# Optimization experiments

Hardware: AMD Instinct MI355X
Metric: run time of the kernel (lower is better)

## Reference

```python
import jax, jax.numpy as jnp
import numpy as np

B, S, DIM, NH = 4, 2048, 2048, 16
HD = DIM // NH  # 128


def setup_inputs() -> dict:
    key = jax.random.key(0)
    ks = jax.random.split(key, 6)
    x = jax.random.normal(ks[0], (B, S, DIM), dtype=jnp.float32)
    wq = jax.random.normal(ks[1], (DIM, DIM), dtype=jnp.float32) * (DIM ** -0.5)
    wk = jax.random.normal(ks[2], (DIM, DIM), dtype=jnp.float32) * (DIM ** -0.5)
    wv = jax.random.normal(ks[3], (DIM, DIM), dtype=jnp.float32) * (DIM ** -0.5)
    wo = jax.random.normal(ks[4], (DIM, DIM), dtype=jnp.float32) * (DIM ** -0.5)
    # RoPE frequencies: theta^{-2i/hd}, angle = pos * freq
    inv_freq = 1.0 / (10000.0 ** (np.arange(0, HD, 2, dtype=np.float32) / HD))  # [HD/2]
    angles = np.arange(S, dtype=np.float32)[:, None] * inv_freq[None, :]  # [S, HD/2]
    freqs_cos = jnp.asarray(np.cos(angles))
    freqs_sin = jnp.asarray(np.sin(angles))
    # causal mask, additive [S, S]
    mask = jnp.where(jnp.tril(jnp.ones((S, S), dtype=bool)), 0.0, -jnp.inf).astype(jnp.float32)
    return {"x": x, "wq": wq, "wk": wk, "wv": wv, "wo": wo,
            "freqs_cos": freqs_cos, "freqs_sin": freqs_sin, "mask": mask,
            "start_pos": 0}


def _apply_rotary(xq, xk, cos, sin):
    # xq, xk: [B, S, H, HD]; cos/sin: [S, HD/2]
    def rot(t):
        tr = t.reshape(*t.shape[:-1], -1, 2)  # [B,S,H,HD/2,2]
        a, b = tr[..., 0], tr[..., 1]
        c = cos[None, :, None, :]
        s = sin[None, :, None, :]
        # complex multiply (a+ib)(c+is)
        out = jnp.stack([a * c - b * s, a * s + b * c], axis=-1)
        return out.reshape(t.shape)
    return rot(xq), rot(xk)


def reference(x, wq, wk, wv, wo, freqs_cos, freqs_sin, mask, start_pos):
    bsz, seqlen, _ = x.shape
    # nn.Linear: y = x @ W^T
    xq = (x @ wq.T).reshape(bsz, seqlen, NH, HD)
    xk = (x @ wk.T).reshape(bsz, seqlen, NH, HD)
    xv = (x @ wv.T).reshape(bsz, seqlen, NH, HD)
    xq, xk = _apply_rotary(xq, xk, freqs_cos, freqs_sin)
    # attention, heads to axis 1
    scores = jnp.einsum('bqhd,bkhd->bhqk', xq, xk) / jnp.sqrt(jnp.float32(HD))
    scores = scores + mask[None, None, :, :]
    probs = jax.nn.softmax(scores.astype(jnp.float32), axis=-1).astype(xq.dtype)
    out = jnp.einsum('bhqk,bkhd->bqhd', probs, xv).reshape(bsz, seqlen, -1)
    return out @ wo.T
```

## Files before the change

### kernel.cpp

```cpp
#include <hip/hip_runtime.h>

typedef __attribute__((ext_vector_type(8))) __bf16 bf16x8;
typedef __attribute__((ext_vector_type(4))) float f32x4;
typedef __attribute__((ext_vector_type(16))) float f32x16;
typedef __attribute__((ext_vector_type(8))) unsigned short u16x8;
typedef __attribute__((ext_vector_type(2))) unsigned uint2v;

#define LOG2E 1.44269504088896340736f

__device__ __forceinline__ unsigned short f2bf(float f){
  union { float f; unsigned u; } v; v.f = f;
  unsigned r = v.u + 0x7FFFu + ((v.u >> 16) & 1u);
  return (unsigned short)(r >> 16);
}
__device__ __forceinline__ float bf2f(unsigned short u){
  union { unsigned u; float f; } v; v.u = ((unsigned)u) << 16;
  return v.f;
}

typedef const unsigned __attribute__((address_space(1)))* gas_ptr;
typedef unsigned __attribute__((address_space(3)))* las_ptr;

__device__ __forceinline__ void gload_lds16(const void* g, void* l){
  __builtin_amdgcn_global_load_lds((gas_ptr)g, (las_ptr)l, 16, 0, 0);
}

__device__ __forceinline__ unsigned cvtpk(float lo, float hi){
  unsigned r;
  asm("v_cvt_pk_bf16_f32 %0, %1, %2" : "=v"(r) : "v"(lo), "v"(hi));
  return r;
}
__device__ __forceinline__ void swap32(unsigned &a, unsigned &b){
  uint2v r = __builtin_amdgcn_permlane32_swap(a, b, false, false);
  a = r[0]; b = r[1];
}

__global__ __launch_bounds__(256) void cvt_f32_bf16(const float* __restrict__ in,
                                                    unsigned short* __restrict__ out){
  size_t i = ((size_t)blockIdx.x * 256 + threadIdx.x) * 4;
  float4 vv = *(const float4*)(in + i);
  ushort4 o;
  o.x = f2bf(vv.x); o.y = f2bf(vv.y); o.z = f2bf(vv.z); o.w = f2bf(vv.w);
  *(ushort4*)(out + i) = o;
}

#define BUF(op, half, par) (LDS + (((op) * 2 + (half)) * 2 + (par)) * 16384)

#define STAGE(op, gbase, half, par, kt) do {                                   \
  _Pragma("unroll")                                                            \
  for (int c_ = 0; c_ < 2; ++c_){                                              \
    int slot_ = c_ * 512 + w * 64 + l;                                         \
    int row_ = slot_ >> 3, colb_ = slot_ & 7;                                  \
    gload_lds16((const char*)((gbase) + (size_t)((half) * 128 + row_) * K +    \
                              (size_t)(kt) * 64 + ((colb_ ^ (row_ & 7)) * 8)), \
                BUF(op, half, par) + c_ * 8192 + w * 1024);                    \
  } } while (0)

#define RD_A(buf) do {                                                         \
  const char* Ab_ = (buf);                                                     \
  _Pragma("unroll")                                                            \
  for (int i_ = 0; i_ < 4; ++i_){                                              \
    int row_ = wm * 64 + i_ * 16 + lq;                                         \
    _Pragma("unroll")                                                          \
    for (int ks_ = 0; ks_ < 2; ++ks_)                                          \
      aA[i_][ks_] = *(const bf16x8*)(Ab_ + row_ * 128 +                        \
                                     (((ks_ * 4 + lg) ^ (row_ & 7)) * 16));    \
  } } while (0)

#define RD_B(buf, arr) do {                                                    \
  const char* Bb_ = (buf);                                                     \
  _Pragma("unroll")                                                            \
  for (int j_ = 0; j_ < 2; ++j_){                                              \
    int row_ = wn * 32 + j_ * 16 + lq;                                         \
    _Pragma("unroll")                                                          \
    for (int ks_ = 0; ks_ < 2; ++ks_)                                          \
      arr[j_][ks_] = *(const bf16x8*)(Bb_ + row_ * 128 +                       \
                                      (((ks_ * 4 + lg) ^ (row_ & 7)) * 16));   \
  } } while (0)

#define DO_MFMA(mh, nh, arr) do {                                              \
  __builtin_amdgcn_s_barrier();                                                \
  asm volatile("s_waitcnt lgkmcnt(0)");                                        \
  __builtin_amdgcn_s_setprio(1);                                               \
  _Pragma("unroll")                                                            \
  for (int i_ = 0; i_ < 4; ++i_)                                               \
    _Pragma("unroll")                                                          \
    for (int j_ = 0; j_ < 2; ++j_)                                             \
      _Pragma("unroll")                                                        \
      for (int ks_ = 0; ks_ < 2; ++ks_)                                        \
        acc[(mh) * 4 + i_][(nh) * 2 + j_] = __builtin_amdgcn_mfma_f32_16x16x32_bf16( \
            aA[i_][ks_], arr[j_][ks_], acc[(mh) * 4 + i_][(nh) * 2 + j_], 0, 0, 0); \
  __builtin_amdgcn_s_setprio(0);                                               \
  __builtin_amdgcn_s_barrier();                                                \
} while (0)

template<bool OUT_BF16, bool ROPE>
__global__ __launch_bounds__(512, 2) void gemm256(const unsigned short* __restrict__ A,
                                                  const unsigned short* __restrict__ B,
                                                  void* __restrict__ Cv,
                                                  int M, int N, int K,
                                                  const float* __restrict__ fc,
                                                  const float* __restrict__ fs){
  __shared__ char LDS[131072];
  const int tid = threadIdx.x;
  const int l = tid & 63, w = tid >> 6;
  const int lq = l & 15, lg = l >> 4;
  const int wm = w >> 2, wn = w & 3;

  const int nwg = gridDim.x, cpx = nwg >> 3;
  const int orig = blockIdx.x;
  const int sw = (orig & 7) * cpx + (orig >> 3);
  const int nbc = N >> 8;
  const int br = sw / nbc, bc = sw % nbc;

  f32x4 acc[8][4] = {};
  bf16x8 aA[4][2], bB0[2][2], bB1[2][2];
  const unsigned short* Ag = A + (size_t)br * 256 * K;
  const unsigned short* Bg = B + (size_t)bc * 256 * K;
  const int NT = K >> 6;

  STAGE(0, Ag, 0, 0, 0); STAGE(1, Bg, 0, 0, 0);
  STAGE(0, Ag, 1, 0, 0); STAGE(1, Bg, 1, 0, 0);
  STAGE(1, Bg, 0, 1, 1); STAGE(0, Ag, 0, 1, 1);
  asm volatile("s_waitcnt vmcnt(4)" ::: "memory");
  __builtin_amdgcn_s_barrier();

  for (int t = 0; t < NT; ++t){
    const int par = t & 1, parn = par ^ 1;
    RD_A(BUF(0, 0, par));
    RD_B(BUF(1, 0, par), bB0);
    if (t + 1 < NT) STAGE(0, Ag, 1, parn, t + 1);
    DO_MFMA(0, 0, bB0);
    RD_B(BUF(1, 1, par), bB1);
    if (t + 1 < NT) STAGE(1, Bg, 1, parn, t + 1);
    DO_MFMA(0, 1, bB1);
    RD_A(BUF(0, 1, par));
    if (t + 2 < NT) STAGE(0, Ag, 0, par, t + 2);
    DO_MFMA(1, 0, bB0);
    if (t + 2 < NT) STAGE(1, Bg, 0, par, t + 2);
    DO_MFMA(1, 1, bB1);
    asm volatile("s_waitcnt vmcnt(4)" ::: "memory");
    __builtin_amdgcn_s_barrier();
  }

#pragma unroll
  for (int i = 0; i < 8; ++i){
    int grow = br * 256 + (i >> 2) * 128 + wm * 64 + (i & 3) * 16 + lg * 4;
#pragma unroll
    for (int j = 0; j < 4; ++j){
      int gcol = bc * 256 + (j >> 1) * 128 + wn * 32 + (j & 1) * 16 + lq;
#pragma unroll
      for (int r = 0; r < 4; ++r){
        float v = acc[i][j][r];
        if (ROPE){
          int s = (grow + r) & 2047;
          int i0 = (gcol & 127) >> 1;
          float cc = fc[s * 64 + i0], sn = fs[s * 64 + i0];
          float part = __shfl_xor(v, 1, 64);
          v = (lq & 1) ? __builtin_fmaf(part, sn, v * cc)
                       : __builtin_fmaf(-part, sn, v * cc);
        }
        if (OUT_BF16)
          ((unsigned short*)Cv)[(size_t)(grow + r) * N + gcol] = f2bf(v);
        else
          ((float*)Cv)[(size_t)(grow + r) * N + gcol] = v;
      }
    }
  }
}

__global__ __launch_bounds__(512, 2) void attn_fwd(const unsigned short* __restrict__ Q,
                                                   const unsigned short* __restrict__ K,
                                                   const unsigned short* __restrict__ V,
                                                   unsigned short* __restrict__ O){
  __shared__ unsigned short SMEM[2 * 64 * 128 + 2 * 128 * 64];
  unsigned short* Ks = SMEM;
  unsigned short* Vt = SMEM + 16384;

  const int tid = threadIdx.x;
  const int l = tid & 63, wid = tid >> 6;
  const int lq = l & 31, hi = l >> 5;
  const int bh = blockIdx.x & 63;
  const int qt = 7 - (blockIdx.x >> 6);
  const int b = bh >> 4, h = bh & 15;
  const int qw = qt * 256 + wid * 32;
  const float c2 = 0.12751743f;

  const unsigned short* qptr = Q + ((size_t)(b * 2048 + qw + lq)) * 2048 + (size_t)h * 128;
  bf16x8 qf[8];
#pragma unroll
  for (int ks = 0; ks < 8; ++ks)
    qf[ks] = *(const bf16x8*)(qptr + ks * 16 + hi * 8);

  f32x16 oacc[4];
#pragma unroll
  for (int i = 0; i < 4; ++i)
#pragma unroll
    for (int j = 0; j < 16; ++j) oacc[i][j] = 0.f;
  float mrow = -3.0e38f, lrow = 0.f;

  const int dblk = tid >> 5, kvp = tid & 31;
  const size_t hb = (size_t)b * 2048 * 2048 + (size_t)h * 128;
  u16x8 r0, r1;

  {
    const size_t kvb = hb;
#pragma unroll
    for (int c = 0; c < 2; ++c){
      int off = c * 8192 + tid * 16;
      int row = off >> 8, colb = off & 255;
      gload_lds16((const char*)(K + kvb + (size_t)row * 2048) + (colb ^ ((row & 15) << 4)),
                  (char*)Ks + c * 8192 + (tid >> 6) * 1024 + (tid & 63) * 16);
    }
    const unsigned short* vp = V + kvb + (size_t)(2 * kvp) * 2048 + dblk * 8;
    r0 = *(const u16x8*)vp; r1 = *(const u16x8*)(vp + 2048);
    asm volatile("s_waitcnt vmcnt(0)" ::: "memory");
#pragma unroll
    for (int j = 0; j < 8; ++j){
      int d = dblk * 8 + j;
      unsigned val = (unsigned)r0[j] | ((unsigned)r1[j] << 16);
      *(unsigned*)((char*)Vt + d * 128 + ((4 * kvp) ^ ((d & 7) << 4))) = val;
    }
  }
  __syncthreads();

  const int nkt = 4 * qt + 4;
  for (int kt = 0; kt < nkt; ++kt){
    const int cur = kt & 1, nxt = cur ^ 1;
    const bool pref = (kt + 1 < nkt);
    char* KsC = (char*)(Ks + cur * 8192);
    char* VtC = (char*)(Vt + cur * 8192);

    if (pref){
      const size_t kvb = hb + (size_t)((kt + 1) * 64) * 2048;
      char* KsN = (char*)(Ks + nxt * 8192);
#pragma unroll
      for (int c = 0; c < 2; ++c){
        int off = c * 8192 + tid * 16;
        int row = off >> 8, colb = off & 255;
        gload_lds16((const char*)(K + kvb + (size_t)row * 2048) + (colb ^ ((row & 15) << 4)),
                    KsN + c * 8192 + (tid >> 6) * 1024 + (tid & 63) * 16);
      }
      const unsigned short* vp = V + kvb + (size_t)(2 * kvp) * 2048 + dblk * 8;
      r0 = *(const u16x8*)vp; r1 = *(const u16x8*)(vp + 2048);
    }

    if (!(kt * 64 > qw + 31)){
      f32x16 sacc[2];
#pragma unroll
      for (int sub = 0; sub < 2; ++sub){
#pragma unroll
        for (int j = 0; j < 16; ++j) sacc[sub][j] = 0.f;
        const int row = sub * 32 + lq;
        const int swz = (row & 15) << 4;
#pragma unroll
        for (int ks = 0; ks < 8; ++ks){
          bf16x8 kf = *(const bf16x8*)(KsC + row * 256 + ((ks * 32 + hi * 16) ^ swz));
          sacc[sub] = __builtin_amdgcn_mfma_f32_32x32x16_bf16(kf, qf[ks], sacc[sub], 0, 0, 0);
        }
      }

      float s[32];
#pragma unroll
      for (int sub = 0; sub < 2; ++sub)
#pragma unroll
        for (int r = 0; r < 16; ++r) s[sub * 16 + r] = sacc[sub][r];

      if (kt * 64 + 63 > qw){
        const int qg = qw + lq;
#pragma unroll
        for (int sub = 0; sub < 2; ++sub)
#pragma unroll
          for (int r = 0; r < 16; ++r){
            int kvg = kt * 64 + sub * 32 + (r & 3) + 8 * (r >> 2) + 4 * hi;
            if (kvg > qg) s[sub * 16 + r] = -3.0e38f;
          }
      }

      float mx[32];
#pragma unroll
      for (int i = 0; i < 32; ++i) mx[i] = s[i];
#pragma unroll
      for (int st = 1; st < 32; st <<= 1)
#pragma unroll
        for (int i = 0; i < 32; i += 2 * st) mx[i] = fmaxf(mx[i], mx[i + st]);
      float pmax = mx[0];
      pmax = fmaxf(pmax, __shfl_xor(pmax, 32, 64));

      float mm;
      if (__all((pmax - mrow) * c2 <= 8.0f)){
        mm = mrow * c2;
      } else {
        float mnew = fmaxf(mrow, pmax);
        mm = mnew * c2;
        float corr = __builtin_amdgcn_exp2f(__builtin_fmaf(mrow, c2, -mm));
        mrow = mnew;
        lrow *= corr;
#pragma unroll
        for (int i = 0; i < 4; ++i)
#pragma unroll
          for (int j = 0; j < 16; ++j) oacc[i][j] *= corr;
      }

      float p[32];
#pragma unroll
      for (int i = 0; i < 32; ++i)
        p[i] = __builtin_amdgcn_exp2f(__builtin_fmaf(s[i], c2, -mm));
      float sm[32];
#pragma unroll
      for (int i = 0; i < 32; ++i) sm[i] = p[i];
#pragma unroll
      for (int st = 1; st < 32; st <<= 1)
#pragma unroll
        for (int i = 0; i < 32; i += 2 * st) sm[i] += sm[i + st];
      float rs = sm[0];
      rs += __shfl_xor(rs, 32, 64);
      lrow += rs;

      unsigned wv[16];
#pragma unroll
      for (int i = 0; i < 16; ++i) wv[i] = cvtpk(p[2 * i], p[2 * i + 1]);
      swap32(wv[0], wv[2]);   swap32(wv[1], wv[3]);
      swap32(wv[4], wv[6]);   swap32(wv[5], wv[7]);
      swap32(wv[8], wv[10]);  swap32(wv[9], wv[11]);
      swap32(wv[12], wv[14]); swap32(wv[13], wv[15]);

#pragma unroll
      for (int c = 0; c < 4; ++c){
        union { unsigned u[4]; bf16x8 v; } pu;
        pu.u[0] = wv[c * 4 + 0]; pu.u[1] = wv[c * 4 + 1];
        pu.u[2] = wv[c * 4 + 2]; pu.u[3] = wv[c * 4 + 3];
#pragma unroll
        for (int db = 0; db < 4; ++db){
          const int d = db * 32 + lq;
          bf16x8 vf = *(const bf16x8*)(VtC + d * 128 + ((c * 32 + hi * 16) ^ ((d & 7) << 4)));
          oacc[db] = __builtin_amdgcn_mfma_f32_32x32x16_bf16(vf, pu.v, oacc[db], 0, 0, 0);
        }
      }
    }

    if (pref){
      asm volatile("s_waitcnt vmcnt(0)" ::: "memory");
      char* VtN = (char*)(Vt + nxt * 8192);
#pragma unroll
      for (int j = 0; j < 8; ++j){
        int d = dblk * 8 + j;
        unsigned val = (unsigned)r0[j] | ((unsigned)r1[j] << 16);
        *(unsigned*)(VtN + d * 128 + ((4 * kvp) ^ ((d & 7) << 4))) = val;
      }
    }
    __syncthreads();
  }

  float inv = 1.0f / lrow;
  char* lb = (char*)SMEM + wid * 8192;
#pragma unroll
  for (int db = 0; db < 4; ++db)
#pragma unroll
    for (int r = 0; r < 16; r += 2){
      int d = db * 32 + (r & 3) + 8 * (r >> 2) + 4 * hi;
      unsigned val = (unsigned)f2bf(oacc[db][r] * inv) |
                     ((unsigned)f2bf(oacc[db][r + 1] * inv) << 16);
      *(unsigned*)(lb + lq * 256 + ((2 * d) ^ ((lq & 7) << 4))) = val;
    }
  __syncthreads();
#pragma unroll
  for (int i = 0; i < 8; ++i){
    int rowq = i * 4 + (l >> 4);
    u16x8 vv = *(const u16x8*)(lb + rowq * 256 + (((l & 15) * 16) ^ ((rowq & 7) << 4)));
    *(u16x8*)(O + ((size_t)(b * 2048 + qw + rowq)) * 2048 + (size_t)h * 128 + (l & 15) * 8) = vv;
  }
}

extern "C" void kernel_launch(void* const* d_in, const int* in_sizes, int n_in,
                              void* d_out, int out_size, void* d_ws, size_t ws_size,
                              hipStream_t stream){
  const float* x  = (const float*)d_in[0];
  const float* wq = (const float*)d_in[1];
  const float* wk = (const float*)d_in[2];
  const float* wv = (const float*)d_in[3];
  const float* wo = (const float*)d_in[4];
  const float* fc = (const float*)d_in[5];
  const float* fs = (const float*)d_in[6];
  float* out = (float*)d_out;
  (void)in_sizes; (void)n_in; (void)out_size; (void)ws_size;

  const size_t XN = (size_t)8192 * 2048;
  const size_t WN = (size_t)2048 * 2048;

  unsigned short* xb  = (unsigned short*)d_ws;
  unsigned short* wqb = xb + XN;
  unsigned short* wkb = wqb + WN;
  unsigned short* wvb = wkb + WN;
  unsigned short* wob = wvb + WN;
  unsigned short* q   = wob + WN;
  unsigned short* k   = q + XN;
  unsigned short* v   = k + XN;
  unsigned short* att = xb;

  cvt_f32_bf16<<<dim3((unsigned)(XN / 1024)), 256, 0, stream>>>(x, xb);
  cvt_f32_bf16<<<dim3((unsigned)(WN / 1024)), 256, 0, stream>>>(wq, wqb);
  cvt_f32_bf16<<<dim3((unsigned)(WN / 1024)), 256, 0, stream>>>(wk, wkb);
  cvt_f32_bf16<<<dim3((unsigned)(WN / 1024)), 256, 0, stream>>>(wv, wvb);
  cvt_f32_bf16<<<dim3((unsigned)(WN / 1024)), 256, 0, stream>>>(wo, wob);

  gemm256<true, true ><<<dim3(256), 512, 0, stream>>>(xb, wqb, q, 8192, 2048, 2048, fc, fs);
  gemm256<true, true ><<<dim3(256), 512, 0, stream>>>(xb, wkb, k, 8192, 2048, 2048, fc, fs);
  gemm256<true, false><<<dim3(256), 512, 0, stream>>>(xb, wvb, v, 8192, 2048, 2048, nullptr, nullptr);

  attn_fwd<<<dim3(512), 512, 0, stream>>>(q, k, v, att);

  gemm256<false, false><<<dim3(256), 512, 0, stream>>>(att, wob, out, 8192, 2048, 2048, nullptr, nullptr);
}
```

Measured before the change: 407.3 us.

## Batch weight casts, reorder attention tiles, and tighten softmax reductions

The four weight fp32-to-bf16 conversions are merged into one launch with a 2D grid, removing three kernel launches. The attention grid mapping now sends half of the blocks heavy-to-light and half light-to-heavy over causal query tiles, to balance work across the machine. The row max uses a shallower 3-way fmax tree, and the cross-half max and sum use permlane32_swap instead of a shuffle. In the GEMM, the trailing vmcnt wait moves inside the last MFMA phase so it shares that phase's closing barrier instead of issuing an extra one.

```diff
diff --git a/kernel.cpp b/kernel.cpp
--- a/kernel.cpp
+++ b/kernel.cpp
@@ -34,9 +34,33 @@
   uint2v r = __builtin_amdgcn_permlane32_swap(a, b, false, false);
   a = r[0]; b = r[1];
 }
+__device__ __forceinline__ float xmax32(float v){
+  union { float f; unsigned u; } a; a.f = v;
+  uint2v r = __builtin_amdgcn_permlane32_swap(a.u, a.u, false, false);
+  union { unsigned u; float f; } x, y; x.u = r[0]; y.u = r[1];
+  return fmaxf(x.f, y.f);
+}
+__device__ __forceinline__ float xsum32(float v){
+  union { float f; unsigned u; } a; a.f = v;
+  uint2v r = __builtin_amdgcn_permlane32_swap(a.u, a.u, false, false);
+  union { unsigned u; float f; } x, y; x.u = r[0]; y.u = r[1];
+  return x.f + y.f;
+}
 
 __global__ __launch_bounds__(256) void cvt_f32_bf16(const float* __restrict__ in,
                                                     unsigned short* __restrict__ out){
+  size_t i = ((size_t)blockIdx.x * 256 + threadIdx.x) * 4;
+  float4 vv = *(const float4*)(in + i);
+  ushort4 o;
+  o.x = f2bf(vv.x); o.y = f2bf(vv.y); o.z = f2bf(vv.z); o.w = f2bf(vv.w);
+  *(ushort4*)(out + i) = o;
+}
+__global__ __launch_bounds__(256) void cvt_w4(const float* __restrict__ w0, const float* __restrict__ w1,
+                                              const float* __restrict__ w2, const float* __restrict__ w3,
+                                              unsigned short* o0, unsigned short* o1,
+                                              unsigned short* o2, unsigned short* o3){
+  const float* in = blockIdx.y == 0 ? w0 : blockIdx.y == 1 ? w1 : blockIdx.y == 2 ? w2 : w3;
+  unsigned short* out = blockIdx.y == 0 ? o0 : blockIdx.y == 1 ? o1 : blockIdx.y == 2 ? o2 : o3;
   size_t i = ((size_t)blockIdx.x * 256 + threadIdx.x) * 4;
   float4 vv = *(const float4*)(in + i);
   ushort4 o;
@@ -78,7 +102,7 @@
                                       (((ks_ * 4 + lg) ^ (row_ & 7)) * 16));   \
   } } while (0)
 
-#define DO_MFMA(mh, nh, arr) do {                                              \
+#define DO_MFMA(mh, nh, arr, tail) do {                                        \
   __builtin_amdgcn_s_barrier();                                                \
   asm volatile("s_waitcnt lgkmcnt(0)");                                        \
   __builtin_amdgcn_s_setprio(1);                                               \
@@ -91,6 +115,7 @@
         acc[(mh) * 4 + i_][(nh) * 2 + j_] = __builtin_amdgcn_mfma_f32_16x16x32_bf16( \
             aA[i_][ks_], arr[j_][ks_], acc[(mh) * 4 + i_][(nh) * 2 + j_], 0, 0, 0); \
   __builtin_amdgcn_s_setprio(0);                                               \
+  tail;                                                                        \
   __builtin_amdgcn_s_barrier();                                                \
 } while (0)
 
@@ -130,17 +155,15 @@
     RD_A(BUF(0, 0, par));
     RD_B(BUF(1, 0, par), bB0);
     if (t + 1 < NT) STAGE(0, Ag, 1, parn, t + 1);
-    DO_MFMA(0, 0, bB0);
+    DO_MFMA(0, 0, bB0, (void)0);
     RD_B(BUF(1, 1, par), bB1);
     if (t + 1 < NT) STAGE(1, Bg, 1, parn, t + 1);
-    DO_MFMA(0, 1, bB1);
+    DO_MFMA(0, 1, bB1, (void)0);
     RD_A(BUF(0, 1, par));
     if (t + 2 < NT) STAGE(0, Ag, 0, par, t + 2);
-    DO_MFMA(1, 0, bB0);
+    DO_MFMA(1, 0, bB0, (void)0);
     if (t + 2 < NT) STAGE(1, Bg, 0, par, t + 2);
-    DO_MFMA(1, 1, bB1);
-    asm volatile("s_waitcnt vmcnt(4)" ::: "memory");
-    __builtin_amdgcn_s_barrier();
+    DO_MFMA(1, 1, bB1, asm volatile("s_waitcnt vmcnt(4)" ::: "memory"));
   }
 
 #pragma unroll
@@ -181,7 +204,9 @@
   const int l = tid & 63, wid = tid >> 6;
   const int lq = l & 31, hi = l >> 5;
   const int bh = blockIdx.x & 63;
-  const int qt = 7 - (blockIdx.x >> 6);
+  const int tsel = blockIdx.x >> 8;
+  const int kidx = (blockIdx.x >> 6) & 3;
+  const int qt = tsel ? kidx : 7 - kidx;
   const int b = bh >> 4, h = bh & 15;
   const int qw = qt * 256 + wid * 32;
   const float c2 = 0.12751743f;
@@ -277,15 +302,17 @@
           }
       }
 
-      float mx[32];
-#pragma unroll
-      for (int i = 0; i < 32; ++i) mx[i] = s[i];
-#pragma unroll
-      for (int st = 1; st < 32; st <<= 1)
-#pragma unroll
-        for (int i = 0; i < 32; i += 2 * st) mx[i] = fmaxf(mx[i], mx[i + st]);
-      float pmax = mx[0];
-      pmax = fmaxf(pmax, __shfl_xor(pmax, 32, 64));
+      float m3[11];
+#pragma unroll
+      for (int i = 0; i < 10; ++i)
+        m3[i] = fmaxf(fmaxf(s[3 * i], s[3 * i + 1]), s[3 * i + 2]);
+      m3[10] = fmaxf(s[30], s[31]);
+      float n0 = fmaxf(fmaxf(m3[0], m3[1]), m3[2]);
+      float n1 = fmaxf(fmaxf(m3[3], m3[4]), m3[5]);
+      float n2 = fmaxf(fmaxf(m3[6], m3[7]), m3[8]);
+      float n3 = fmaxf(m3[9], m3[10]);
+      float pmax = fmaxf(fmaxf(n0, n1), fmaxf(n2, n3));
+      pmax = xmax32(pmax);
 
       float mm;
       if (__all((pmax - mrow) * c2 <= 8.0f)){
@@ -313,9 +340,7 @@
       for (int st = 1; st < 32; st <<= 1)
 #pragma unroll
         for (int i = 0; i < 32; i += 2 * st) sm[i] += sm[i + st];
-      float rs = sm[0];
-      rs += __shfl_xor(rs, 32, 64);
-      lrow += rs;
+      lrow += xsum32(sm[0]);
 
       unsigned wv[16];
 #pragma unroll
@@ -399,10 +424,7 @@
   unsigned short* att = xb;
 
   cvt_f32_bf16<<<dim3((unsigned)(XN / 1024)), 256, 0, stream>>>(x, xb);
-  cvt_f32_bf16<<<dim3((unsigned)(WN / 1024)), 256, 0, stream>>>(wq, wqb);
-  cvt_f32_bf16<<<dim3((unsigned)(WN / 1024)), 256, 0, stream>>>(wk, wkb);
-  cvt_f32_bf16<<<dim3((unsigned)(WN / 1024)), 256, 0, stream>>>(wv, wvb);
-  cvt_f32_bf16<<<dim3((unsigned)(WN / 1024)), 256, 0, stream>>>(wo, wob);
+  cvt_w4<<<dim3((unsigned)(WN / 1024), 4), 256, 0, stream>>>(wq, wk, wv, wo, wqb, wkb, wvb, wob);
 
   gemm256<true, true ><<<dim3(256), 512, 0, stream>>>(xb, wqb, q, 8192, 2048, 2048, fc, fs);
   gemm256<true, true ><<<dim3(256), 512, 0, stream>>>(xb, wkb, k, 8192, 2048, 2048, fc, fs);
```

Measured after the change: 401.2 us. Within noise of the previous version (-1.5%).
